# Performance work log

Measured on AMD Instinct MI355X. Metric: run time of the kernel, lower is better.

Reference implementation:

```python
import jax, jax.numpy as jnp
import numpy as np

BLOCK_M = 64
BLOCK_K = 64
THRES = 0.8


def setup_inputs() -> dict:
    key = jax.random.key(0)
    k1, k2 = jax.random.split(key)
    bsz, d_in, d_out = 8192, 4096, 4096
    x = jax.random.normal(k1, (bsz, d_in), dtype=jnp.float32)
    # kaiming_uniform_(a=sqrt(5)) on a (d_in, d_out) tensor -> bound = 1/sqrt(d_out)
    bound = 1.0 / np.sqrt(d_out)
    weight = jax.random.uniform(k2, (d_in, d_out), dtype=jnp.float32,
                                minval=-bound, maxval=bound)
    return {"x": x, "weight": weight}


def reference(x, weight):
    bsz, hidden = x.shape
    nm, nk = bsz // BLOCK_M, hidden // BLOCK_K
    # per-block average magnitude of activations: [nm, nk]
    blocks = jnp.abs(x).reshape(nm, BLOCK_M, nk, BLOCK_K)
    avg_mag = blocks.mean(axis=(1, 3))
    block_mask = avg_mag > THRES  # [nm, nk] bool
    # expand mask to element level and zero inactive activation blocks
    mask_elem = jnp.repeat(jnp.repeat(block_mask, BLOCK_M, axis=0), BLOCK_K, axis=1)
    x_masked = jnp.where(mask_elem, x, 0.0)
    # block-sparse masked GEMM (dense reference of the same math)
    return x_masked @ weight
```

## Files before the change

kernel.cpp:

```cpp
#include <hip/hip_runtime.h>
#include <hip/hip_bf16.h>
#include <stdint.h>

#define BSZ   8192
#define D_IN  4096
#define D_OUT 4096
#define NM    128
#define NK    64

typedef __bf16 bf16x8 __attribute__((ext_vector_type(8)));
typedef float  f32x4  __attribute__((ext_vector_type(4)));
typedef unsigned short ushort_t;

__device__ __forceinline__ ushort_t f2bf(float f) {
  union { __hip_bfloat16 h; ushort_t u; } c;
  c.h = __float2bfloat16(f);
  return c.u;
}

__device__ __forceinline__ bf16x8 ld_frag(const ushort_t* p) {
  union { uint4 u; bf16x8 b; } cv;
  cv.u = *(const uint4*)p;
  return cv.b;
}

__device__ __forceinline__ void glds16(const ushort_t* g, ushort_t* l) {
  __builtin_amdgcn_global_load_lds(
      (const __attribute__((address_space(1))) unsigned int*)g,
      (__attribute__((address_space(3))) unsigned int*)l,
      16, 0, 0);
}

__global__ __launch_bounds__(256) void mask_cast_kernel(
    const float* __restrict__ x, ushort_t* __restrict__ xb,
    int* __restrict__ mask) {
  const int kblk = blockIdx.x;
  const int mblk = blockIdx.y;
  const int tid  = threadIdx.x;
  const int lane = tid & 63;
  const int wv   = tid >> 6;
  const size_t row0 = (size_t)mblk * 64;
  const int    col0 = kblk * 64;

  float4 v[4];
  double s = 0.0;
#pragma unroll
  for (int i = 0; i < 4; ++i) {
    int j = i * 256 + tid;
    int r = j >> 4;
    int c = (j & 15) * 4;
    v[i] = *(const float4*)(x + (row0 + r) * D_IN + col0 + c);
    s += (double)fabsf(v[i].x) + (double)fabsf(v[i].y) +
         (double)fabsf(v[i].z) + (double)fabsf(v[i].w);
  }

#pragma unroll
  for (int off = 32; off > 0; off >>= 1) {
    union { double d; int i2[2]; } u;
    u.d = s;
    u.i2[0] = __shfl_xor(u.i2[0], off, 64);
    u.i2[1] = __shfl_xor(u.i2[1], off, 64);
    s += u.d;
  }

  __shared__ double wsum[4];
  __shared__ int mflag;
  if (lane == 0) wsum[wv] = s;
  __syncthreads();
  if (tid == 0) {
    double tot = wsum[0] + wsum[1] + wsum[2] + wsum[3];
    float avg = (float)(tot * (1.0 / 4096.0));
    int m = (avg > 0.8f) ? 1 : 0;
    mflag = m;
    mask[mblk * NK + kblk] = m;
  }
  __syncthreads();

  if (mflag) {
#pragma unroll
    for (int i = 0; i < 4; ++i) {
      int j = i * 256 + tid;
      int r = j >> 4;
      int c = (j & 15) * 4;
      ushort4 o = make_ushort4(f2bf(v[i].x), f2bf(v[i].y),
                               f2bf(v[i].z), f2bf(v[i].w));
      *(ushort4*)(xb + (row0 + r) * D_IN + col0 + c) = o;
    }
  }
}

__global__ __launch_bounds__(256) void wcast_transpose_kernel(
    const float* __restrict__ w, ushort_t* __restrict__ wT) {
  const int ntile = blockIdx.x;
  const int ktile = blockIdx.y;
  const int tid   = threadIdx.x;
  const int k0 = ktile * 64, n0 = ntile * 64;

  __shared__ ushort_t t[64][65];

#pragma unroll
  for (int i = 0; i < 4; ++i) {
    int j = i * 256 + tid;
    int r = j >> 4;
    int c = (j & 15) * 4;
    float4 v = *(const float4*)(w + (size_t)(k0 + r) * D_OUT + n0 + c);
    t[r][c + 0] = f2bf(v.x);
    t[r][c + 1] = f2bf(v.y);
    t[r][c + 2] = f2bf(v.z);
    t[r][c + 3] = f2bf(v.w);
  }
  __syncthreads();
#pragma unroll
  for (int i = 0; i < 4; ++i) {
    int j = i * 256 + tid;
    int r = j >> 4;
    int c = (j & 15) * 4;
    ushort4 o = make_ushort4(t[c + 0][r], t[c + 1][r], t[c + 2][r], t[c + 3][r]);
    *(ushort4*)(wT + (size_t)(n0 + r) * D_IN + k0 + c) = o;
  }
}

__global__ __launch_bounds__(256) void bsp_gemm_kernel(
    const ushort_t* __restrict__ xb, const ushort_t* __restrict__ wT,
    const int* __restrict__ mask, float* __restrict__ out) {
  const int ntile = blockIdx.x;
  const int mblk  = blockIdx.y;
  const int tid   = threadIdx.x;
  const int lane  = tid & 63;
  const int wv    = tid >> 6;
  const int m0 = mblk * 64;
  const int n0 = ntile * 256;

  __shared__ ushort_t As[64 * 64];
  __shared__ ushort_t Bs[256 * 64];
  __shared__ int nact;
  __shared__ unsigned char klist[64];

  const int* mrow = mask + mblk * NK;
  if (tid == 0) {
    int n = 0;
#pragma unroll
    for (int kb = 0; kb < NK; ++kb) {
      if (mrow[kb] != 0) klist[n++] = (unsigned char)kb;
    }
    nact = n;
  }
  __syncthreads();
  const int na = nact;

  f32x4 acc[4][4] = {};

  const int lr  = lane >> 3;
  const int lcs = ((lane & 7) ^ (lane >> 3)) * 8;
  const int q   = lane >> 4;
  const int l15 = lane & 15;
  const int sx  = l15 & 7;

  for (int ki = 0; ki < na; ++ki) {
    const int kb = klist[ki];
    const int k0 = kb * 64;

#pragma unroll
    for (int t = 0; t < 2; ++t) {
      int rb = wv * 16 + t * 8;
      glds16(xb + (size_t)(m0 + rb + lr) * D_IN + k0 + lcs, &As[rb * 64]);
    }
#pragma unroll
    for (int t = 0; t < 8; ++t) {
      int rb = wv * 64 + t * 8;
      glds16(wT + (size_t)(n0 + rb + lr) * D_IN + k0 + lcs, &Bs[rb * 64]);
    }
    __syncthreads();

#pragma unroll
    for (int c = 0; c < 2; ++c) {
      const int sw = ((c * 4 + q) ^ sx) * 8;
      bf16x8 a[4], b[4];
#pragma unroll
      for (int i = 0; i < 4; ++i)
        a[i] = ld_frag(&As[(i * 16 + l15) * 64 + sw]);
#pragma unroll
      for (int j = 0; j < 4; ++j)
        b[j] = ld_frag(&Bs[(wv * 64 + j * 16 + l15) * 64 + sw]);
#pragma unroll
      for (int i = 0; i < 4; ++i)
#pragma unroll
        for (int j = 0; j < 4; ++j)
          acc[i][j] = __builtin_amdgcn_mfma_f32_16x16x32_bf16(
              a[i], b[j], acc[i][j], 0, 0, 0);
    }
    __syncthreads();
  }

#pragma unroll
  for (int i = 0; i < 4; ++i) {
#pragma unroll
    for (int j = 0; j < 4; ++j) {
#pragma unroll
      for (int r = 0; r < 4; ++r) {
        int row = m0 + i * 16 + q * 4 + r;
        int col = n0 + wv * 64 + j * 16 + l15;
        out[(size_t)row * D_OUT + col] = acc[i][j][r];
      }
    }
  }
}

extern "C" void kernel_launch(void* const* d_in, const int* in_sizes, int n_in,
                              void* d_out, int out_size, void* d_ws, size_t ws_size,
                              hipStream_t stream) {
  const float* x = (const float*)d_in[0];
  const float* w = (const float*)d_in[1];

  ushort_t* xb  = (ushort_t*)d_ws;
  ushort_t* wT  = (ushort_t*)((char*)d_ws + (size_t)BSZ * D_IN * 2);
  int*      msk = (int*)((char*)d_ws + (size_t)BSZ * D_IN * 2 + (size_t)D_IN * D_OUT * 2);
  float*    out = (float*)d_out;

  hipLaunchKernelGGL(mask_cast_kernel, dim3(NK, NM), dim3(256), 0, stream,
                     x, xb, msk);
  hipLaunchKernelGGL(wcast_transpose_kernel, dim3(64, 64), dim3(256), 0, stream,
                     w, wT);
  hipLaunchKernelGGL(bsp_gemm_kernel, dim3(D_OUT / 256, NM), dim3(256), 0, stream,
                     xb, wT, msk, out);
}
```

Before: 440.6 us.

## Pair two M-blocks per workgroup to share B tiles over union of active k-blocks

The GEMM workgroup now covers 128 rows (two mask row-blocks) with 8 waves, loading each weight tile once for both halves. It iterates over the union of the two rows' active k-blocks, and waves skip the A load and MFMAs when their half is inactive. The active-list build switches from a serial scan by one thread to a wave ballot plus prefix popcount. This cuts weight-tile reloads, but it adds loop iterations where half the waves sit idle at barriers and uses more LDS per workgroup.

```diff
diff --git a/kernel.cpp b/kernel.cpp
--- a/kernel.cpp
+++ b/kernel.cpp
@@ -120,30 +120,34 @@
   }
 }
 
-__global__ __launch_bounds__(256) void bsp_gemm_kernel(
+__global__ __launch_bounds__(512) void bsp_gemm_kernel(
     const ushort_t* __restrict__ xb, const ushort_t* __restrict__ wT,
     const int* __restrict__ mask, float* __restrict__ out) {
   const int ntile = blockIdx.x;
-  const int mblk  = blockIdx.y;
+  const int mpair = blockIdx.y;
   const int tid   = threadIdx.x;
   const int lane  = tid & 63;
   const int wv    = tid >> 6;
-  const int m0 = mblk * 64;
+  const int mi    = wv >> 2;
+  const int nj    = wv & 3;
+  const int m0 = mpair * 128;
   const int n0 = ntile * 256;
 
-  __shared__ ushort_t As[64 * 64];
+  __shared__ ushort_t As[128 * 64];
   __shared__ ushort_t Bs[256 * 64];
   __shared__ int nact;
   __shared__ unsigned char klist[64];
 
-  const int* mrow = mask + mblk * NK;
-  if (tid == 0) {
-    int n = 0;
-#pragma unroll
-    for (int kb = 0; kb < NK; ++kb) {
-      if (mrow[kb] != 0) klist[n++] = (unsigned char)kb;
-    }
-    nact = n;
+  if (tid < 64) {
+    const int* mrow = mask + (size_t)(mpair * 2) * NK;
+    int a0 = (mrow[tid] != 0) ? 1 : 0;
+    int a1 = (mrow[NK + tid] != 0) ? 1 : 0;
+    unsigned long long u = __ballot(a0 | a1);
+    if (a0 | a1) {
+      int pos = __popcll(u & ((1ull << tid) - 1ull));
+      klist[pos] = (unsigned char)(tid | (a0 << 6) | (a1 << 7));
+    }
+    if (tid == 0) nact = (int)__popcll(u);
   }
   __syncthreads();
   const int na = nact;
@@ -157,37 +161,43 @@
   const int sx  = l15 & 7;
 
   for (int ki = 0; ki < na; ++ki) {
-    const int kb = klist[ki];
-    const int k0 = kb * 64;
-
-#pragma unroll
-    for (int t = 0; t < 2; ++t) {
-      int rb = wv * 16 + t * 8;
-      glds16(xb + (size_t)(m0 + rb + lr) * D_IN + k0 + lcs, &As[rb * 64]);
-    }
-#pragma unroll
-    for (int t = 0; t < 8; ++t) {
-      int rb = wv * 64 + t * 8;
+    const int e   = klist[ki];
+    const int kb  = e & 63;
+    const int k0  = kb * 64;
+    const int act = (e >> (6 + mi)) & 1;
+
+    if (act) {
+#pragma unroll
+      for (int t = 0; t < 2; ++t) {
+        int rb = wv * 16 + t * 8;
+        glds16(xb + (size_t)(m0 + rb + lr) * D_IN + k0 + lcs, &As[rb * 64]);
+      }
+    }
+#pragma unroll
+    for (int t = 0; t < 4; ++t) {
+      int rb = wv * 32 + t * 8;
       glds16(wT + (size_t)(n0 + rb + lr) * D_IN + k0 + lcs, &Bs[rb * 64]);
     }
     __syncthreads();
 
-#pragma unroll
-    for (int c = 0; c < 2; ++c) {
-      const int sw = ((c * 4 + q) ^ sx) * 8;
-      bf16x8 a[4], b[4];
-#pragma unroll
-      for (int i = 0; i < 4; ++i)
-        a[i] = ld_frag(&As[(i * 16 + l15) * 64 + sw]);
-#pragma unroll
-      for (int j = 0; j < 4; ++j)
-        b[j] = ld_frag(&Bs[(wv * 64 + j * 16 + l15) * 64 + sw]);
-#pragma unroll
-      for (int i = 0; i < 4; ++i)
+    if (act) {
+#pragma unroll
+      for (int c = 0; c < 2; ++c) {
+        const int sw = ((c * 4 + q) ^ sx) * 8;
+        bf16x8 a[4], b[4];
+#pragma unroll
+        for (int i = 0; i < 4; ++i)
+          a[i] = ld_frag(&As[(mi * 64 + i * 16 + l15) * 64 + sw]);
 #pragma unroll
         for (int j = 0; j < 4; ++j)
-          acc[i][j] = __builtin_amdgcn_mfma_f32_16x16x32_bf16(
-              a[i], b[j], acc[i][j], 0, 0, 0);
+          b[j] = ld_frag(&Bs[(nj * 64 + j * 16 + l15) * 64 + sw]);
+#pragma unroll
+        for (int i = 0; i < 4; ++i)
+#pragma unroll
+          for (int j = 0; j < 4; ++j)
+            acc[i][j] = __builtin_amdgcn_mfma_f32_16x16x32_bf16(
+                a[i], b[j], acc[i][j], 0, 0, 0);
+      }
     }
     __syncthreads();
   }
@@ -198,8 +208,8 @@
     for (int j = 0; j < 4; ++j) {
 #pragma unroll
       for (int r = 0; r < 4; ++r) {
-        int row = m0 + i * 16 + q * 4 + r;
-        int col = n0 + wv * 64 + j * 16 + l15;
+        int row = m0 + mi * 64 + i * 16 + q * 4 + r;
+        int col = n0 + nj * 64 + j * 16 + l15;
         out[(size_t)row * D_OUT + col] = acc[i][j][r];
       }
     }
@@ -221,6 +231,6 @@
                      x, xb, msk);
   hipLaunchKernelGGL(wcast_transpose_kernel, dim3(64, 64), dim3(256), 0, stream,
                      w, wT);
-  hipLaunchKernelGGL(bsp_gemm_kernel, dim3(D_OUT / 256, NM), dim3(256), 0, stream,
+  hipLaunchKernelGGL(bsp_gemm_kernel, dim3(D_OUT / 256, NM / 2), dim3(512), 0, stream,
                      xb, wT, msk, out);
 }
```

New measurement: 421.3 us. 1.05x faster.
